# Kernel optimization log

Measured on AMD Instinct MI355X. Metric: run time of the kernel, lower is better.

## Reference

```python
import jax, jax.numpy as jnp
import numpy as np

B = 1024        # batch
C = 256         # channels (nodes)
ORDER = 4       # power-series order
DIM = C * (C - 1) // 2  # number of node pairs (edges)
LEAKY_SLOPE = 0.01      # torch nn.LeakyReLU default


def _diff_matrix():
    # column e corresponds to pair (p, q), p < q: diff = x_p - x_q
    p, q = np.triu_indices(C, k=1)
    D = np.zeros((C, DIM), dtype=np.float32)
    e = np.arange(DIM)
    D[p, e] = 1.0
    D[q, e] = -1.0
    return jnp.asarray(D)


def setup_inputs() -> dict:
    key = jax.random.key(0)
    k1, k2 = jax.random.split(key, 2)
    x = jax.random.normal(k1, (B, C), dtype=jnp.float32)
    w1 = jnp.ones((C,), dtype=jnp.float32)            # DiagonalLinear init: zeros + 1
    w2 = jax.random.normal(k2, (ORDER,), dtype=jnp.float32) * 0.1  # Grandson_net Linear(order,1) weight
    w3 = jnp.ones((DIM,), dtype=jnp.float32)          # DiagonalLinear on dim
    return {"x": x, "w1": w1, "w2": w2, "w3": w3, "diff_indices": _diff_matrix()}


def reference(x, w1, w2, w3, diff_indices):
    # fc1: diagonal scaling (the original wastes a full matmul on diag_embed)
    o1 = x * w1                                   # [B, C]
    diffs = o1 @ diff_indices                     # [B, DIM] pairwise differences
    sign = jnp.sign(diffs)
    a = jnp.abs(diffs)
    # power series a^1 .. a^ORDER (original stacks then loops Grandson_net per dim;
    # the Linear(order,1) is shared, so it is a single contraction over ORDER)
    pows = jnp.stack([a ** (i + 1) for i in range(ORDER)], axis=2)  # [B, DIM, ORDER]
    o3 = jax.nn.leaky_relu(jnp.einsum('bdo,o->bd', pows, w2), LEAKY_SLOPE)
    o3 = o3 * sign * w3                           # restore sign, fc3 diagonal scale
    # node aggregation: out[:, i] = -sum_{e: i is + end} o3[:, e] + sum_{e: i is - end} o3[:, e]
    # which is exactly -o3 @ diff_indices^T
    out = -(o3 @ diff_indices.T)                  # [B, C]
    return out[..., None]                         # [B, C, 1]
```

## Files before the change

kernel.cpp:

```cpp
#include <hip/hip_runtime.h>


#define C_NODES 256
#define BT      64
#define PADC    260
#define NW      8

__global__ __launch_bounds__(512, 4) void son_kernel(
    const float* __restrict__ x, const float* __restrict__ w1,
    const float* __restrict__ w2, const float* __restrict__ w3,
    float* __restrict__ out)
{
    __shared__ __align__(16) float o1t[BT * PADC];
    __shared__ __align__(16) float wrow[NW * C_NODES];

    const int t    = threadIdx.x;
    const int lane = t & 63;
    const int w    = t >> 6;
    const int b0   = blockIdx.x * BT;
    const int i    = __builtin_amdgcn_readfirstlane(blockIdx.y * NW + w);

    {
        const int c4 = lane * 4;
        const float4 w1v = *(const float4*)&w1[c4];
        #pragma unroll
        for (int rr = 0; rr < BT / NW; ++rr) {
            const int row = w + NW * rr;
            const float4 xv = *(const float4*)&x[(b0 + row) * C_NODES + c4];
            float4 o;
            o.x = xv.x * w1v.x; o.y = xv.y * w1v.y;
            o.z = xv.z * w1v.z; o.w = xv.w * w1v.w;
            *(float4*)&o1t[row * PADC + c4] = o;
        }
    }

    {
        const int j0 = lane * 4;
        float4 wv;
        #pragma unroll
        for (int k = 0; k < 4; ++k) {
            const int j = j0 + k;
            const int p = (i < j) ? i : j;
            const int q = (i < j) ? j : i;
            const int e = (i == j) ? 0 : (p * (511 - p)) / 2 + q - p - 1;
            ((float*)&wv)[k] = -w3[e];
        }
        *(float4*)&wrow[w * C_NODES + j0] = wv;
    }
    __syncthreads();

    const float c0 = w2[0], c1 = w2[1], c2 = w2[2], c3 = w2[3];
    const float oi = o1t[lane * PADC + i];
    float acc = 0.f;

    #pragma unroll 4
    for (int jg = 0; jg < C_NODES / 4; ++jg) {
        const float4 ov = *(const float4*)&o1t[lane * PADC + 4 * jg];
        const float4 wv = *(const float4*)&wrow[w * C_NODES + 4 * jg];
        #pragma unroll
        for (int k = 0; k < 4; ++k) {
            const float oj = ((const float*)&ov)[k];
            const float wk = ((const float*)&wv)[k];
            const float d  = oi - oj;
            const float a  = fabsf(d);
            const float t3 = __builtin_fmaf(a,
                               __builtin_fmaf(a,
                                 __builtin_fmaf(a, c3, c2), c1), c0);
            const float u   = d * t3;
            const float sel = (t3 > 0.f) ? 1.0f : 0.01f;
            acc = __builtin_fmaf(u * sel, wk, acc);
        }
    }

    out[(b0 + lane) * C_NODES + i] = acc;
}

extern "C" void kernel_launch(void* const* d_in, const int* in_sizes, int n_in,
                              void* d_out, int out_size, void* d_ws, size_t ws_size,
                              hipStream_t stream) {
    const float* x  = (const float*)d_in[0];
    const float* w1 = (const float*)d_in[1];
    const float* w2 = (const float*)d_in[2];
    const float* w3 = (const float*)d_in[3];
    float* out = (float*)d_out;

    const int B = in_sizes[0] / C_NODES;
    dim3 grid(B / BT, C_NODES / NW);
    son_kernel<<<grid, 512, 0, stream>>>(x, w1, w2, w3, out);
}
```

Baseline: 21.65 us.

## Compute two output nodes per wave and swizzle shared-memory layout

Each wave now handles two output nodes i, so each o1t float4 loaded from LDS is reused for two computations. Blocks shrink to 256 threads, and the o1t padding is replaced by an XOR swizzle to avoid bank conflicts. The leaky-relu select is rewritten as fmaxf(t3, 0.01*t3). Costs are more registers per thread and fewer waves per block, which may lower occupancy or latency hiding.

```diff
diff --git a/kernel.cpp b/kernel.cpp
--- a/kernel.cpp
+++ b/kernel.cpp
@@ -3,76 +3,101 @@
 
 #define C_NODES 256
 #define BT      64
-#define PADC    260
-#define NW      8
+#define NW      4
+#define RPW     2
+#define NPB     (NW*RPW)
 
-__global__ __launch_bounds__(512, 4) void son_kernel(
+__global__ __launch_bounds__(256, 2) void son_kernel(
     const float* __restrict__ x, const float* __restrict__ w1,
     const float* __restrict__ w2, const float* __restrict__ w3,
     float* __restrict__ out)
 {
-    __shared__ __align__(16) float o1t[BT * PADC];
-    __shared__ __align__(16) float wrow[NW * C_NODES];
+    __shared__ __align__(16) float o1t[BT * C_NODES];
+    __shared__ __align__(16) float wrow[NPB * C_NODES];
 
-    const int t    = threadIdx.x;
-    const int lane = t & 63;
-    const int w    = t >> 6;
-    const int b0   = blockIdx.x * BT;
-    const int i    = __builtin_amdgcn_readfirstlane(blockIdx.y * NW + w);
+    const int t  = threadIdx.x;
+    const int b0 = blockIdx.x * BT;
 
     {
-        const int c4 = lane * 4;
+        const int chunk = t & 63;
+        const int c4    = chunk << 2;
         const float4 w1v = *(const float4*)&w1[c4];
         #pragma unroll
-        for (int rr = 0; rr < BT / NW; ++rr) {
-            const int row = w + NW * rr;
+        for (int p = 0; p < 16; ++p) {
+            const int row = (t >> 6) + (p << 2);
             const float4 xv = *(const float4*)&x[(b0 + row) * C_NODES + c4];
             float4 o;
             o.x = xv.x * w1v.x; o.y = xv.y * w1v.y;
             o.z = xv.z * w1v.z; o.w = xv.w * w1v.w;
-            *(float4*)&o1t[row * PADC + c4] = o;
+            const int phys = chunk ^ (row & 7);
+            *(float4*)&o1t[(row << 8) + (phys << 2)] = o;
         }
     }
 
     {
-        const int j0 = lane * 4;
-        float4 wv;
+        const int lane = t & 63;
+        const int wv_  = t >> 6;
         #pragma unroll
-        for (int k = 0; k < 4; ++k) {
-            const int j = j0 + k;
-            const int p = (i < j) ? i : j;
-            const int q = (i < j) ? j : i;
-            const int e = (i == j) ? 0 : (p * (511 - p)) / 2 + q - p - 1;
-            ((float*)&wv)[k] = -w3[e];
+        for (int rr = 0; rr < RPW; ++rr) {
+            const int r = wv_ * RPW + rr;
+            const int i = blockIdx.y * NPB + r;
+            float4 wv;
+            #pragma unroll
+            for (int k = 0; k < 4; ++k) {
+                const int j = lane * 4 + k;
+                const int p = (i < j) ? i : j;
+                const int q = (i < j) ? j : i;
+                ((float*)&wv)[k] = (i == j) ? 0.f
+                                 : -w3[(p * (511 - p)) / 2 + q - p - 1];
+            }
+            *(float4*)&wrow[(r << 8) + (lane << 2)] = wv;
         }
-        *(float4*)&wrow[w * C_NODES + j0] = wv;
     }
     __syncthreads();
 
+    const int lane    = t & 63;
+    const int w       = __builtin_amdgcn_readfirstlane(t >> 6);
+    const int r0      = w * RPW;
+    const int i0      = blockIdx.y * NPB + r0;
+    const int swz     = lane & 7;
+    const int rowbase = lane << 8;
+
     const float c0 = w2[0], c1 = w2[1], c2 = w2[2], c3 = w2[3];
-    const float oi = o1t[lane * PADC + i];
-    float acc = 0.f;
+
+    const float oi0 = o1t[rowbase + ((((i0 >> 2) ^ swz) << 2) | (i0 & 3))];
+    const float oi1 = o1t[rowbase + (((((i0 + 1) >> 2) ^ swz) << 2) | ((i0 + 1) & 3))];
+
+    float acc0 = 0.f, acc1 = 0.f;
 
     #pragma unroll 4
-    for (int jg = 0; jg < C_NODES / 4; ++jg) {
-        const float4 ov = *(const float4*)&o1t[lane * PADC + 4 * jg];
-        const float4 wv = *(const float4*)&wrow[w * C_NODES + 4 * jg];
+    for (int jc = 0; jc < 64; ++jc) {
+        const float4 ov = *(const float4*)&o1t[rowbase + ((jc ^ swz) << 2)];
+        const float4 wa = *(const float4*)&wrow[(r0 << 8) + (jc << 2)];
+        const float4 wb = *(const float4*)&wrow[((r0 + 1) << 8) + (jc << 2)];
         #pragma unroll
         for (int k = 0; k < 4; ++k) {
             const float oj = ((const float*)&ov)[k];
-            const float wk = ((const float*)&wv)[k];
-            const float d  = oi - oj;
-            const float a  = fabsf(d);
-            const float t3 = __builtin_fmaf(a,
-                               __builtin_fmaf(a,
-                                 __builtin_fmaf(a, c3, c2), c1), c0);
-            const float u   = d * t3;
-            const float sel = (t3 > 0.f) ? 1.0f : 0.01f;
-            acc = __builtin_fmaf(u * sel, wk, acc);
+            {
+                const float d   = oi0 - oj;
+                const float a   = fabsf(d);
+                const float t3  = __builtin_fmaf(a, __builtin_fmaf(a,
+                                    __builtin_fmaf(a, c3, c2), c1), c0);
+                const float t3s = fmaxf(t3, 0.01f * t3);
+                acc0 = __builtin_fmaf(d * t3s, ((const float*)&wa)[k], acc0);
+            }
+            {
+                const float d   = oi1 - oj;
+                const float a   = fabsf(d);
+                const float t3  = __builtin_fmaf(a, __builtin_fmaf(a,
+                                    __builtin_fmaf(a, c3, c2), c1), c0);
+                const float t3s = fmaxf(t3, 0.01f * t3);
+                acc1 = __builtin_fmaf(d * t3s, ((const float*)&wb)[k], acc1);
+            }
         }
     }
 
-    out[(b0 + lane) * C_NODES + i] = acc;
+    out[(b0 + lane) * C_NODES + i0]     = acc0;
+    out[(b0 + lane) * C_NODES + i0 + 1] = acc1;
 }
 
 extern "C" void kernel_launch(void* const* d_in, const int* in_sizes, int n_in,
@@ -85,6 +110,6 @@
     float* out = (float*)d_out;
 
     const int B = in_sizes[0] / C_NODES;
-    dim3 grid(B / BT, C_NODES / NW);
-    son_kernel<<<grid, 512, 0, stream>>>(x, w1, w2, w3, out);
+    dim3 grid(B / BT, C_NODES / NPB);
+    son_kernel<<<grid, 256, 0, stream>>>(x, w1, w2, w3, out);
 }
```

New measurement: 22.61 us. +4.4%, slower.

## Remap threads to node pairs with per-batch accumulators and LDS reduction

Applied to the files above, without the earlier changes.

Work is reassigned so each wave owns two output nodes and each lane covers four j-columns across a 32-row batch tile. The w3 row weights now live in registers instead of LDS, and partial sums are reduced through LDS and cross-lane shuffles. Each oi value is reused for two nodes, and the branchy leaky-relu select is replaced with fmaxf(t3, 0.01*t3). The change adds a reduction phase and 64 accumulator registers per thread, which may hurt occupancy.

```diff
diff --git a/kernel.cpp b/kernel.cpp
--- a/kernel.cpp
+++ b/kernel.cpp
@@ -2,77 +2,99 @@
 
 
 #define C_NODES 256
-#define BT      64
-#define PADC    260
+#define BT      32
 #define NW      8
+#define NPB     16
 
 __global__ __launch_bounds__(512, 4) void son_kernel(
     const float* __restrict__ x, const float* __restrict__ w1,
     const float* __restrict__ w2, const float* __restrict__ w3,
     float* __restrict__ out)
 {
-    __shared__ __align__(16) float o1t[BT * PADC];
-    __shared__ __align__(16) float wrow[NW * C_NODES];
+    __shared__ __align__(16) float o1t[8704];
 
     const int t    = threadIdx.x;
     const int lane = t & 63;
     const int w    = t >> 6;
     const int b0   = blockIdx.x * BT;
-    const int i    = __builtin_amdgcn_readfirstlane(blockIdx.y * NW + w);
+    const int i0   = blockIdx.y * NPB + 2 * w;
+
+    float4 wv0, wv1;
+    #pragma unroll
+    for (int k = 0; k < 4; ++k) {
+        const int j = 4 * lane + k;
+        {   const int p = (i0 < j) ? i0 : j, q = (i0 < j) ? j : i0;
+            ((float*)&wv0)[k] = (i0 == j) ? 0.f
+                               : -w3[(p * (511 - p)) / 2 + q - p - 1]; }
+        {   const int i1 = i0 + 1;
+            const int p = (i1 < j) ? i1 : j, q = (i1 < j) ? j : i1;
+            ((float*)&wv1)[k] = (i1 == j) ? 0.f
+                               : -w3[(p * (511 - p)) / 2 + q - p - 1]; }
+    }
 
     {
-        const int c4 = lane * 4;
+        const int c4 = lane << 2;
         const float4 w1v = *(const float4*)&w1[c4];
         #pragma unroll
-        for (int rr = 0; rr < BT / NW; ++rr) {
-            const int row = w + NW * rr;
-            const float4 xv = *(const float4*)&x[(b0 + row) * C_NODES + c4];
+        for (int p = 0; p < 4; ++p) {
+            const int r = w + (p << 3);
+            const float4 xv = *(const float4*)&x[(b0 + r) * C_NODES + c4];
             float4 o;
             o.x = xv.x * w1v.x; o.y = xv.y * w1v.y;
             o.z = xv.z * w1v.z; o.w = xv.w * w1v.w;
-            *(float4*)&o1t[row * PADC + c4] = o;
+            *(float4*)&o1t[(r << 8) + c4] = o;
         }
-    }
-
-    {
-        const int j0 = lane * 4;
-        float4 wv;
-        #pragma unroll
-        for (int k = 0; k < 4; ++k) {
-            const int j = j0 + k;
-            const int p = (i < j) ? i : j;
-            const int q = (i < j) ? j : i;
-            const int e = (i == j) ? 0 : (p * (511 - p)) / 2 + q - p - 1;
-            ((float*)&wv)[k] = -w3[e];
-        }
-        *(float4*)&wrow[w * C_NODES + j0] = wv;
     }
     __syncthreads();
 
     const float c0 = w2[0], c1 = w2[1], c2 = w2[2], c3 = w2[3];
-    const float oi = o1t[lane * PADC + i];
-    float acc = 0.f;
+    const int l4 = lane << 2;
 
-    #pragma unroll 4
-    for (int jg = 0; jg < C_NODES / 4; ++jg) {
-        const float4 ov = *(const float4*)&o1t[lane * PADC + 4 * jg];
-        const float4 wv = *(const float4*)&wrow[w * C_NODES + 4 * jg];
+    float2 acc[BT];
+    #pragma unroll
+    for (int b = 0; b < BT; ++b) { acc[b].x = 0.f; acc[b].y = 0.f; }
+
+    #pragma unroll
+    for (int b = 0; b < BT; ++b) {
+        const float4 ov = *(const float4*)&o1t[(b << 8) + l4];
+        const float2 oi = *(const float2*)&o1t[(b << 8) + i0];
         #pragma unroll
         for (int k = 0; k < 4; ++k) {
             const float oj = ((const float*)&ov)[k];
-            const float wk = ((const float*)&wv)[k];
-            const float d  = oi - oj;
-            const float a  = fabsf(d);
-            const float t3 = __builtin_fmaf(a,
-                               __builtin_fmaf(a,
-                                 __builtin_fmaf(a, c3, c2), c1), c0);
-            const float u   = d * t3;
-            const float sel = (t3 > 0.f) ? 1.0f : 0.01f;
-            acc = __builtin_fmaf(u * sel, wk, acc);
+            {   const float d = oi.x - oj, a = fabsf(d);
+                const float t3 = __builtin_fmaf(a, __builtin_fmaf(a,
+                                   __builtin_fmaf(a, c3, c2), c1), c0);
+                acc[b].x = __builtin_fmaf(d * fmaxf(t3, 0.01f * t3),
+                                          ((const float*)&wv0)[k], acc[b].x); }
+            {   const float d = oi.y - oj, a = fabsf(d);
+                const float t3 = __builtin_fmaf(a, __builtin_fmaf(a,
+                                   __builtin_fmaf(a, c3, c2), c1), c0);
+                acc[b].y = __builtin_fmaf(d * fmaxf(t3, 0.01f * t3),
+                                          ((const float*)&wv1)[k], acc[b].y); }
         }
     }
 
-    out[(b0 + lane) * C_NODES + i] = acc;
+    __syncthreads();
+    float* red = &o1t[w * 1088];
+    #pragma unroll
+    for (int r = 0; r < 4; ++r) {
+        #pragma unroll
+        for (int bb = 0; bb < 8; ++bb) {
+            red[(bb * 2 + 0) * 68 + lane] = acc[r * 8 + bb].x;
+            red[(bb * 2 + 1) * 68 + lane] = acc[r * 8 + bb].y;
+        }
+        float s = 0.f;
+        const int base = (lane & 15) * 68 + ((lane >> 4) << 4);
+        #pragma unroll
+        for (int c = 0; c < 4; ++c) {
+            const float4 v = *(const float4*)&red[base + (c << 2)];
+            s += (v.x + v.y) + (v.z + v.w);
+        }
+        s += __shfl_xor(s, 16, 64);
+        s += __shfl_xor(s, 32, 64);
+        if (lane < 16)
+            out[(b0 + r * 8 + (lane >> 1)) * C_NODES + i0 + (lane & 1)] = s;
+    }
 }
 
 extern "C" void kernel_launch(void* const* d_in, const int* in_sizes, int n_in,
@@ -85,6 +107,6 @@
     float* out = (float*)d_out;
 
     const int B = in_sizes[0] / C_NODES;
-    dim3 grid(B / BT, C_NODES / NW);
+    dim3 grid(B / BT, C_NODES / NPB);
     son_kernel<<<grid, 512, 0, stream>>>(x, w1, w2, w3, out);
 }
```

Result: slower. 23.82 us (+10.0%).
